# Performance work log

Hardware: AMD Instinct MI355X
Metric: run time of the kernel (lower is better)

## Reference

```python
import jax, jax.numpy as jnp
import numpy as np

H, DQS, DQP, DVS, DVP = 12, 16, 4, 16, 8
S_SCALAR = (3.0 * DQS) ** -0.5
S_POINT = (3.0 * DQP * (9.0 * 2.0 ** 0.5)) ** -0.5
S_PAIR = 3.0 ** -0.5
_OFF = np.cumsum([0, H * DQS, H * DQS, H * DVS, H * DQP * 3, H * DQP * 3, H * DVP * 3])


def _ln(x, g, b, eps=1e-5):
    mu = x.mean(-1, keepdims=True)
    var = x.var(-1, keepdims=True)
    return (x - mu) / jnp.sqrt(var + eps) * g + b


def setup_inputs() -> dict:
    B, N, D, PD = 2, 512, 384, 128
    key = jax.random.key(0)
    ks = jax.random.split(key, 12)
    node_feats = jax.random.normal(ks[0], (B, N, D), jnp.float32)
    pair_feats = jax.random.normal(ks[1], (B, N, N, PD), jnp.float32)
    mask = jnp.ones((B, N), dtype=bool)
    # random per-residue rigid frames (orthonormal rotations via QR)
    rot = jnp.linalg.qr(jax.random.normal(ks[2], (B, N, 3, 3), jnp.float32))[0]
    trans = jax.random.normal(ks[3], (B, N, 3), jnp.float32)
    dim_qkv = int(_OFF[-1])             # 1152
    dim_out = H * (PD + DVS + 4 * DVP)  # 2112
    s = 0.02
    p = dict(
        ln_s_g=jnp.ones((D,)), ln_s_b=jnp.zeros((D,)),
        ln_p_g=jnp.ones((PD,)), ln_p_b=jnp.zeros((PD,)),
        w_pair_bias=s * jax.random.normal(ks[4], (PD, H), jnp.float32),
        w_qkv=s * jax.random.normal(ks[5], (D, dim_qkv), jnp.float32),
        point_weights=jnp.full((1, H, 1, 1), float(np.log(np.e - 1.0)), jnp.float32),
        w_out=s * jax.random.normal(ks[6], (dim_out, D), jnp.float32),
        b_out=jnp.zeros((D,)),
        ln_t_g=jnp.ones((D,)), ln_t_b=jnp.zeros((D,)),
        w_ff1=s * jax.random.normal(ks[7], (D, 4 * D), jnp.float32),
        b_ff1=jnp.zeros((4 * D,)),
        w_ff2=s * jax.random.normal(ks[8], (4 * D, D), jnp.float32),
        b_ff2=jnp.zeros((D,)),
    )
    return dict(node_feats=node_feats, pair_feats=pair_feats, mask=mask,
                rot=rot, trans=trans, **p)


def reference(node_feats, pair_feats, mask, rot, trans,
              ln_s_g, ln_s_b, ln_p_g, ln_p_b, w_pair_bias, w_qkv,
              point_weights, w_out, b_out,
              ln_t_g, ln_t_b, w_ff1, b_ff1, w_ff2, b_ff2):
    b, n, d = node_feats.shape
    x = _ln(node_feats, ln_s_g, ln_s_b)
    p = _ln(pair_feats, ln_p_g, ln_p_b)
    pair_bias = jnp.einsum('bijd,dh->bhij', p, w_pair_bias)
    qkv = x @ w_qkv  # (b,n,1152)

    def heads(t, dh):
        return t.reshape(b, n, H, dh).transpose(0, 2, 1, 3)  # b h n d

    q_s = heads(qkv[..., _OFF[0]:_OFF[1]], DQS)
    k_s = heads(qkv[..., _OFF[1]:_OFF[2]], DQS)
    v_s = heads(qkv[..., _OFF[2]:_OFF[3]], DVS)

    def to_pts(t, dp):
        pts = t.reshape(b, n, H * dp, 3)
        # rigid apply: R_i @ x + t_i (global frame)
        pts = jnp.einsum('bnxy,bnpy->bnpx', rot, pts) + trans[:, :, None, :]
        return pts.reshape(b, n, H, dp, 3).transpose(0, 2, 1, 3, 4)  # b h n d 3

    q_p = to_pts(qkv[..., _OFF[3]:_OFF[4]], DQP)
    k_p = to_pts(qkv[..., _OFF[4]:_OFF[5]], DQP)
    v_p = to_pts(qkv[..., _OFF[5]:_OFF[6]], DVP)

    scalar_logits = jnp.einsum('bhid,bhjd->bhij', q_s, k_s)
    # dist attn: -sum_{d,c} (q-k)^2, expanded to avoid (b,h,n,n,d,3) intermediate
    qq = jnp.sum(q_p * q_p, axis=(-1, -2))
    kk = jnp.sum(k_p * k_p, axis=(-1, -2))
    qk = jnp.einsum('bhidc,bhjdc->bhij', q_p, k_p)
    point_logits = -(qq[..., :, None] + kk[..., None, :] - 2.0 * qk)
    point_logits = point_logits * jax.nn.softplus(point_weights)

    neg = jnp.finfo(node_feats.dtype).min
    pm = mask[:, None, :, None] & mask[:, None, None, :]  # b 1 i j
    scalar_logits = jnp.where(pm, scalar_logits, neg)
    point_logits = jnp.where(pm, point_logits, neg)
    pair_bias = jnp.where(pm, pair_bias, neg)

    logits = S_SCALAR * scalar_logits + S_POINT * point_logits + S_PAIR * pair_bias
    attn = jax.nn.softmax(logits, axis=-1)

    out_s = jnp.einsum('bhij,bhjd->bhid', attn, v_s)
    out_pair = jnp.einsum('bhij,bijd->bhid', attn, p)
    out_p = jnp.einsum('bhij,bhjdc->bhidc', attn, v_p)
    # rigid inverse: R_i^T (x - t_i) back to local frame
    pts = out_p.transpose(0, 2, 1, 3, 4).reshape(b, n, H * DVP, 3)
    pts = jnp.einsum('bnyx,bnpy->bnpx', rot, pts - trans[:, :, None, :])
    out_p = pts.reshape(b, n, H, DVP, 3)
    pnorm = jnp.sqrt(jnp.sum(out_p * out_p, axis=-1) + 1e-8)  # safe_norm

    cat = jnp.concatenate([
        out_s.transpose(0, 2, 1, 3).reshape(b, n, H * DVS),
        out_p.reshape(b, n, H * DVP * 3),
        pnorm.reshape(b, n, H * DVP),
        out_pair.transpose(0, 2, 1, 3).reshape(b, n, -1),
    ], axis=-1)
    attn_out = cat @ w_out + b_out

    # residuals + transition (dropout=0 -> identity). Note: transition is
    # applied to attn_out (pre-residual), exactly as in the torch forward.
    node1 = attn_out + node_feats
    t = _ln(attn_out, ln_t_g, ln_t_b)
    t = jax.nn.gelu(t @ w_ff1 + b_ff1) @ w_ff2 + b_ff2
    return t + node1
```

## Files before the change

### kernel.cpp

```cpp
#include <hip/hip_runtime.h>
#include <hip/hip_bf16.h>
#include <math.h>

typedef __hip_bfloat16 bf16;
typedef _Float16 f16;
typedef unsigned short ushort_t;
typedef ushort_t ushort8 __attribute__((ext_vector_type(8)));
typedef ushort_t us4 __attribute__((ext_vector_type(4)));
typedef short bf16x8 __attribute__((ext_vector_type(8)));
typedef f16 f16x8 __attribute__((ext_vector_type(8)));
typedef float f32x4 __attribute__((ext_vector_type(4)));

constexpr float S_SCALAR = 0.14433756729740643f;
constexpr float S_POINT  = 0.08091531528f;
constexpr float S_PAIR   = 0.5773502691896258f;

__device__ inline float ldf(const float* p) { return *p; }
__device__ inline void stf(float* p, float v) { *p = v; }

__device__ inline short f2bfs(float x) {
  return (short)__builtin_bit_cast(unsigned short, __float2bfloat16(x));
}
__device__ inline ushort_t f2bfu(float x) {
  return (ushort_t)__builtin_bit_cast(unsigned short, __float2bfloat16(x));
}
__device__ inline ushort_t f2hu(float x) {
  return __builtin_bit_cast(ushort_t, (f16)x);
}
__device__ inline float h2f(ushort_t u) {
  return (float)__builtin_bit_cast(f16, u);
}

__device__ inline float gelu_tanh(float x) {
  float c = 0.7978845608028654f * (x + 0.044715f * x * x * x);
  return 0.5f * x * (1.f + tanhf(c));
}

__global__ __launch_bounds__(128) void ln384_kernel(
    const float* __restrict__ in, const float* __restrict__ g,
    const float* __restrict__ b, float* __restrict__ out)
{
  int row = blockIdx.x;
  const float* x = in + (size_t)row * 384;
  int t = threadIdx.x;
  float v[3]; float s = 0.f, s2 = 0.f;
#pragma unroll
  for (int i = 0; i < 3; i++) { v[i] = x[t + 128 * i]; s += v[i]; s2 += v[i] * v[i]; }
  for (int o = 32; o; o >>= 1) { s += __shfl_down(s, o); s2 += __shfl_down(s2, o); }
  __shared__ float sh[4];
  int wid = t >> 6, lane = t & 63;
  if (lane == 0) { sh[wid] = s; sh[2 + wid] = s2; }
  __syncthreads();
  s = sh[0] + sh[1]; s2 = sh[2] + sh[3];
  float mean = s * (1.f / 384.f);
  float var = s2 * (1.f / 384.f) - mean * mean;
  float rstd = rsqrtf(fmaxf(var, 0.f) + 1e-5f);
  float* orow = out + (size_t)row * 384;
#pragma unroll
  for (int i = 0; i < 3; i++) {
    int c = t + 128 * i;
    orow[c] = (v[i] - mean) * rstd * g[c] + b[c];
  }
}

__global__ __launch_bounds__(256) void prep_all_kernel(
    const float* __restrict__ w_qkv, const float* __restrict__ w_out,
    const float* __restrict__ w_ff1, const float* __restrict__ w_ff2,
    ushort_t* __restrict__ wqkvT, ushort_t* __restrict__ woutT,
    ushort_t* __restrict__ wff1T, ushort_t* __restrict__ wff2T,
    const float* __restrict__ g, const float* __restrict__ bb,
    const float* __restrict__ wpb, ushort_t* __restrict__ gwbT,
    float* __restrict__ gsbs,
    const float* __restrict__ node, const float* __restrict__ ln_s_g,
    const float* __restrict__ ln_s_b, float* __restrict__ xout)
{
  __shared__ float shmem[2048];
  int bid = blockIdx.x;
  int t = threadIdx.x;
  if (bid < 2376) {
    const float* src; ushort_t* dst; int K, N, bx, by;
    if (bid < 432)       { src = w_qkv; dst = wqkvT; K = 384;  N = 1152; bx = bid % 36;          by = bid / 36; }
    else if (bid < 1224) { src = w_out; dst = woutT; K = 2112; N = 384;  bx = (bid - 432) % 12;  by = (bid - 432) / 12; }
    else if (bid < 1800) { src = w_ff1; dst = wff1T; K = 384;  N = 1536; bx = (bid - 1224) % 48; by = (bid - 1224) / 48; }
    else                 { src = w_ff2; dst = wff2T; K = 1536; N = 384;  bx = (bid - 1800) % 12; by = (bid - 1800) / 12; }
    float (&tile)[32][33] = *reinterpret_cast<float (*)[32][33]>(shmem);
    int n0 = bx * 32, k0 = by * 32;
    int c = t & 31, r4 = (t >> 5) * 4;
#pragma unroll
    for (int i = 0; i < 4; i++)
      tile[r4 + i][c] = src[(size_t)(k0 + r4 + i) * N + n0 + c];
    __syncthreads();
#pragma unroll
    for (int i = 0; i < 4; i++)
      dst[(size_t)(n0 + r4 + i) * K + k0 + c] = f2bfu(tile[c][r4 + i]);
    return;
  }
  if (bid == 2376) {
    for (int idx = t; idx < 2048; idx += 256) {
      int h = idx >> 7, c = idx & 127;
      float v = (h < 12) ? g[c] * wpb[c * 12 + h] : 0.f;
      bf16 r = __float2bfloat16(v);
      gwbT[idx] = __builtin_bit_cast(unsigned short, r);
      shmem[idx] = __bfloat162float(r);
    }
    __syncthreads();
    if (t < 16) {
      float s = 0.f;
      for (int c = 0; c < 128; c++) s += shmem[t * 128 + c];
      gsbs[t] = s;
    } else if (t < 32) {
      int h = t - 16;
      float s = 0.f;
      if (h < 12) for (int c = 0; c < 128; c++) s = fmaf(bb[c], wpb[c * 12 + h], s);
      gsbs[t] = s;
    }
    return;
  }
  int half = t >> 7, tt = t & 127;
  int row = (bid - 2377) * 2 + half;
  const float* x = node + (size_t)row * 384;
  float v[3]; float s = 0.f, s2 = 0.f;
#pragma unroll
  for (int i = 0; i < 3; i++) { v[i] = x[tt + 128 * i]; s += v[i]; s2 += v[i] * v[i]; }
  for (int o = 32; o; o >>= 1) { s += __shfl_down(s, o); s2 += __shfl_down(s2, o); }
  int wid = t >> 6, lane = t & 63;
  if (lane == 0) { shmem[wid] = s; shmem[4 + wid] = s2; }
  __syncthreads();
  s = shmem[half * 2] + shmem[half * 2 + 1];
  s2 = shmem[4 + half * 2] + shmem[4 + half * 2 + 1];
  float mean = s * (1.f / 384.f);
  float var = s2 * (1.f / 384.f) - mean * mean;
  float rstd = rsqrtf(fmaxf(var, 0.f) + 1e-5f);
  float* orow = xout + (size_t)row * 384;
#pragma unroll
  for (int i = 0; i < 3; i++) {
    int c = tt + 128 * i;
    orow[c] = (v[i] - mean) * rstd * ln_s_g[c] + ln_s_b[c];
  }
}

template <int EPI>
__global__ __launch_bounds__(256) void gemm_mfma_kernel(
    const float* __restrict__ A, const ushort_t* __restrict__ BT,
    const float* __restrict__ bias, const float* __restrict__ r1,
    const float* __restrict__ r2, float* __restrict__ C,
    int M, int Nn, int K)
{
  __shared__ ushort_t As[64][72];
  __shared__ ushort_t Bs[64][72];
  int t = threadIdx.x;
  int w = t >> 6, l = t & 63;
  int m0 = blockIdx.y * 64, n0 = blockIdx.x * 64;
  int wm = (w >> 1) * 32, wn = (w & 1) * 32;
  int lr = l & 15, lk = l >> 4;
  int sr = t >> 2, sc = (t & 3) * 16;
  f32x4 acc[2][2];
#pragma unroll
  for (int i = 0; i < 2; i++)
#pragma unroll
    for (int j = 0; j < 2; j++) acc[i][j] = (f32x4){0.f, 0.f, 0.f, 0.f};

  for (int k0 = 0; k0 < K; k0 += 64) {
    const float* Ar = A + (size_t)(m0 + sr) * K + k0 + sc;
    const ushort_t* Br = BT + (size_t)(n0 + sr) * K + k0 + sc;
    float4 a0 = *(const float4*)(Ar + 0);
    float4 a1 = *(const float4*)(Ar + 4);
    float4 a2 = *(const float4*)(Ar + 8);
    float4 a3 = *(const float4*)(Ar + 12);
    ushort8 b0 = *(const ushort8*)(Br + 0);
    ushort8 b1 = *(const ushort8*)(Br + 8);
    ushort8 u0, u1;
    u0[0] = f2bfu(a0.x); u0[1] = f2bfu(a0.y); u0[2] = f2bfu(a0.z); u0[3] = f2bfu(a0.w);
    u0[4] = f2bfu(a1.x); u0[5] = f2bfu(a1.y); u0[6] = f2bfu(a1.z); u0[7] = f2bfu(a1.w);
    u1[0] = f2bfu(a2.x); u1[1] = f2bfu(a2.y); u1[2] = f2bfu(a2.z); u1[3] = f2bfu(a2.w);
    u1[4] = f2bfu(a3.x); u1[5] = f2bfu(a3.y); u1[6] = f2bfu(a3.z); u1[7] = f2bfu(a3.w);
    *(ushort8*)&As[sr][sc] = u0;
    *(ushort8*)&As[sr][sc + 8] = u1;
    *(ushort8*)&Bs[sr][sc] = b0;
    *(ushort8*)&Bs[sr][sc + 8] = b1;
    __syncthreads();
#pragma unroll
    for (int kk = 0; kk < 2; kk++) {
      bf16x8 af0 = *(const bf16x8*)&As[wm + lr][kk * 32 + lk * 8];
      bf16x8 af1 = *(const bf16x8*)&As[wm + 16 + lr][kk * 32 + lk * 8];
      bf16x8 bf0 = *(const bf16x8*)&Bs[wn + lr][kk * 32 + lk * 8];
      bf16x8 bf1 = *(const bf16x8*)&Bs[wn + 16 + lr][kk * 32 + lk * 8];
      acc[0][0] = __builtin_amdgcn_mfma_f32_16x16x32_bf16(af0, bf0, acc[0][0], 0, 0, 0);
      acc[0][1] = __builtin_amdgcn_mfma_f32_16x16x32_bf16(af0, bf1, acc[0][1], 0, 0, 0);
      acc[1][0] = __builtin_amdgcn_mfma_f32_16x16x32_bf16(af1, bf0, acc[1][0], 0, 0, 0);
      acc[1][1] = __builtin_amdgcn_mfma_f32_16x16x32_bf16(af1, bf1, acc[1][1], 0, 0, 0);
    }
    __syncthreads();
  }
#pragma unroll
  for (int mf = 0; mf < 2; mf++) {
#pragma unroll
    for (int nf = 0; nf < 2; nf++) {
      int nn = n0 + wn + nf * 16 + lr;
      float bv = bias ? bias[nn] : 0.f;
#pragma unroll
      for (int e = 0; e < 4; e++) {
        int m = m0 + wm + mf * 16 + lk * 4 + e;
        float v = acc[mf][nf][e] + bv;
        if (EPI == 1) v = gelu_tanh(v);
        if (EPI == 2) v += r1[(size_t)m * Nn + nn] + r2[(size_t)m * Nn + nn];
        C[(size_t)m * Nn + nn] = v;
      }
    }
  }
}

__global__ __launch_bounds__(256) void qkv_post_kernel(
    const float* __restrict__ qkv, const float* __restrict__ rot,
    const float* __restrict__ trans, const float* __restrict__ pw,
    f16* __restrict__ qhat, f16* __restrict__ khat,
    float* __restrict__ kkb, ushort_t* __restrict__ vT)
{
  int bh = blockIdx.x;
  int b = bh / 12, h = bh - b * 12;
  int j = blockIdx.y * 256 + threadIdx.x;
  int bn = b * 512 + j;
  const float* row = qkv + (size_t)bn * 1152;
  float R[9];
#pragma unroll
  for (int k = 0; k < 9; k++) R[k] = rot[bn * 9 + k];
  float T0 = trans[bn * 3], T1 = trans[bn * 3 + 1], T2 = trans[bn * 3 + 2];
  float sp = log1pf(__expf(pw[h]));
  float c1 = 2.f * S_POINT * sp;
  f16* qh = qhat + ((size_t)bh * 512 + j) * 32;
  f16* kh = khat + ((size_t)bh * 512 + j) * 32;
#pragma unroll
  for (int d = 0; d < 16; d++) {
    qh[d] = (f16)(S_SCALAR * row[h * 16 + d]);
    kh[d] = (f16)(row[192 + h * 16 + d]);
  }
#pragma unroll
  for (int p = 0; p < 4; p++) {
    int base = 576 + (h * 4 + p) * 3;
    float x = row[base], y = row[base + 1], z = row[base + 2];
    qh[16 + p * 3 + 0] = (f16)(c1 * (R[0] * x + R[1] * y + R[2] * z + T0));
    qh[16 + p * 3 + 1] = (f16)(c1 * (R[3] * x + R[4] * y + R[5] * z + T1));
    qh[16 + p * 3 + 2] = (f16)(c1 * (R[6] * x + R[7] * y + R[8] * z + T2));
  }
  float kksum = 0.f;
#pragma unroll
  for (int p = 0; p < 4; p++) {
    int base = 720 + (h * 4 + p) * 3;
    float x = row[base], y = row[base + 1], z = row[base + 2];
    float gx = R[0] * x + R[1] * y + R[2] * z + T0;
    float gy = R[3] * x + R[4] * y + R[5] * z + T1;
    float gz = R[6] * x + R[7] * y + R[8] * z + T2;
    kh[16 + p * 3 + 0] = (f16)gx; kh[16 + p * 3 + 1] = (f16)gy; kh[16 + p * 3 + 2] = (f16)gz;
    kksum = fmaf(gx, gx, kksum); kksum = fmaf(gy, gy, kksum); kksum = fmaf(gz, gz, kksum);
  }
#pragma unroll
  for (int d = 28; d < 32; d++) { qh[d] = (f16)0.f; kh[d] = (f16)0.f; }
  kkb[(size_t)bh * 512 + j] = kksum;
  ushort_t* vt = vT + (size_t)bh * 40 * 512;
#pragma unroll
  for (int c = 0; c < 16; c++) vt[c * 512 + j] = f2hu(row[384 + h * 16 + c]);
#pragma unroll
  for (int p = 0; p < 8; p++) {
    int base = 864 + (h * 8 + p) * 3;
    float x = row[base], y = row[base + 1], z = row[base + 2];
    vt[(16 + p * 3 + 0) * 512 + j] = f2hu(R[0] * x + R[1] * y + R[2] * z + T0);
    vt[(16 + p * 3 + 1) * 512 + j] = f2hu(R[3] * x + R[4] * y + R[5] * z + T1);
    vt[(16 + p * 3 + 2) * 512 + j] = f2hu(R[6] * x + R[7] * y + R[8] * z + T2);
  }
}

__global__ __launch_bounds__(256) void pair_bias_kernel(
    const float* __restrict__ pair, const ushort_t* __restrict__ gwbT,
    const float* __restrict__ gsbs, const float* __restrict__ g,
    const float* __restrict__ bb, ushort_t* __restrict__ bias,
    f16* __restrict__ pnT)
{
  int t = threadIdx.x;
  int wv = t >> 6, l = t & 63;
  int lr = l & 15, lk = l >> 4;
  size_t rid0 = (size_t)blockIdx.x * 128 + (size_t)wv * 32;

  bf16x8 bfrag[4];
#pragma unroll
  for (int kc = 0; kc < 4; kc++) {
    const ushort_t* gp = gwbT + lr * 128 + kc * 32 + lk * 8;
    us4 q0 = *(const us4*)gp;
    us4 q1 = *(const us4*)(gp + 4);
    bfrag[kc][0] = (short)q0[0]; bfrag[kc][1] = (short)q0[1];
    bfrag[kc][2] = (short)q0[2]; bfrag[kc][3] = (short)q0[3];
    bfrag[kc][4] = (short)q1[0]; bfrag[kc][5] = (short)q1[1];
    bfrag[kc][6] = (short)q1[2]; bfrag[kc][7] = (short)q1[3];
  }

  const float* p0 = pair + (rid0 + lr) * 128 + lk * 8;
  f32x4 acc0 = {0.f, 0.f, 0.f, 0.f}, acc1 = {0.f, 0.f, 0.f, 0.f};
  float s0 = 0.f, s20 = 0.f, s1 = 0.f, s21 = 0.f;
#pragma unroll
  for (int kc = 0; kc < 4; kc++) {
    float4 u0 = *(const float4*)(p0 + kc * 32);
    float4 u1 = *(const float4*)(p0 + kc * 32 + 4);
    float4 w0 = *(const float4*)(p0 + 2048 + kc * 32);
    float4 w1 = *(const float4*)(p0 + 2048 + kc * 32 + 4);
    s0 += u0.x + u0.y + u0.z + u0.w + u1.x + u1.y + u1.z + u1.w;
    s20 = fmaf(u0.x, u0.x, s20); s20 = fmaf(u0.y, u0.y, s20);
    s20 = fmaf(u0.z, u0.z, s20); s20 = fmaf(u0.w, u0.w, s20);
    s20 = fmaf(u1.x, u1.x, s20); s20 = fmaf(u1.y, u1.y, s20);
    s20 = fmaf(u1.z, u1.z, s20); s20 = fmaf(u1.w, u1.w, s20);
    s1 += w0.x + w0.y + w0.z + w0.w + w1.x + w1.y + w1.z + w1.w;
    s21 = fmaf(w0.x, w0.x, s21); s21 = fmaf(w0.y, w0.y, s21);
    s21 = fmaf(w0.z, w0.z, s21); s21 = fmaf(w0.w, w0.w, s21);
    s21 = fmaf(w1.x, w1.x, s21); s21 = fmaf(w1.y, w1.y, s21);
    s21 = fmaf(w1.z, w1.z, s21); s21 = fmaf(w1.w, w1.w, s21);
    bf16x8 a0, a1;
    a0[0] = f2bfs(u0.x); a0[1] = f2bfs(u0.y); a0[2] = f2bfs(u0.z); a0[3] = f2bfs(u0.w);
    a0[4] = f2bfs(u1.x); a0[5] = f2bfs(u1.y); a0[6] = f2bfs(u1.z); a0[7] = f2bfs(u1.w);
    a1[0] = f2bfs(w0.x); a1[1] = f2bfs(w0.y); a1[2] = f2bfs(w0.z); a1[3] = f2bfs(w0.w);
    a1[4] = f2bfs(w1.x); a1[5] = f2bfs(w1.y); a1[6] = f2bfs(w1.z); a1[7] = f2bfs(w1.w);
    acc0 = __builtin_amdgcn_mfma_f32_16x16x32_bf16(a0, bfrag[kc], acc0, 0, 0, 0);
    acc1 = __builtin_amdgcn_mfma_f32_16x16x32_bf16(a1, bfrag[kc], acc1, 0, 0, 0);
  }
  s0 += __shfl_xor(s0, 16);  s0 += __shfl_xor(s0, 32);
  s20 += __shfl_xor(s20, 16); s20 += __shfl_xor(s20, 32);
  s1 += __shfl_xor(s1, 16);  s1 += __shfl_xor(s1, 32);
  s21 += __shfl_xor(s21, 16); s21 += __shfl_xor(s21, 32);
  float mean0 = s0 * (1.f / 128.f);
  float rstd0 = rsqrtf(fmaxf(s20 * (1.f / 128.f) - mean0 * mean0, 0.f) + 1e-5f);
  float mean1 = s1 * (1.f / 128.f);
  float rstd1 = rsqrtf(fmaxf(s21 * (1.f / 128.f) - mean1 * mean1, 0.f) + 1e-5f);

  int slab = (int)(rid0 >> 9);
  int j0w = (int)(rid0 & 511);
  f16* sl = pnT + (size_t)slab * 65536;
  int ju = j0w + lr, jw = j0w + 16 + lr;
#pragma unroll
  for (int kc = 0; kc < 4; kc++) {
    int c0 = kc * 32 + lk * 8;
    float4 u0 = *(const float4*)(p0 + kc * 32);
    float4 u1 = *(const float4*)(p0 + kc * 32 + 4);
    float4 w0 = *(const float4*)(p0 + 2048 + kc * 32);
    float4 w1 = *(const float4*)(p0 + 2048 + kc * 32 + 4);
    float4 g0 = *(const float4*)(g + c0);
    float4 g1 = *(const float4*)(g + c0 + 4);
    float4 b0 = *(const float4*)(bb + c0);
    float4 b1 = *(const float4*)(bb + c0 + 4);
    float uu[8] = {u0.x, u0.y, u0.z, u0.w, u1.x, u1.y, u1.z, u1.w};
    float ww[8] = {w0.x, w0.y, w0.z, w0.w, w1.x, w1.y, w1.z, w1.w};
    float gg[8] = {g0.x, g0.y, g0.z, g0.w, g1.x, g1.y, g1.z, g1.w};
    float bv[8] = {b0.x, b0.y, b0.z, b0.w, b1.x, b1.y, b1.z, b1.w};
#pragma unroll
    for (int e = 0; e < 8; e++) {
      sl[(size_t)(c0 + e) * 512 + ju] = (f16)(fmaf((uu[e] - mean0) * rstd0, gg[e], bv[e]));
      sl[(size_t)(c0 + e) * 512 + jw] = (f16)(fmaf((ww[e] - mean1) * rstd1, gg[e], bv[e]));
    }
  }

  float gsum = gsbs[lr], bsum = gsbs[16 + lr];
  int b = (int)(rid0 >> 18);
  int i = (int)((rid0 >> 9) & 511);
  int j0 = (int)(rid0 & 511);
  us4 pk0, pk1;
#pragma unroll
  for (int e = 0; e < 4; e++) {
    int r = lk * 4 + e;
    float m0 = __shfl(mean0, r), rs0 = __shfl(rstd0, r);
    float m1 = __shfl(mean1, r), rs1 = __shfl(rstd1, r);
    pk0[e] = f2hu(rs0 * (acc0[e] - m0 * gsum) + bsum);
    pk1[e] = f2hu(rs1 * (acc1[e] - m1 * gsum) + bsum);
  }
  if (lr < 12) {
    ushort_t* dst = bias + ((size_t)(b * 12 + lr) * 512 + i) * 512 + j0 + lk * 4;
    *(us4*)dst = pk0;
    *(us4*)(dst + 16) = pk1;
  }
}

__global__ __launch_bounds__(256, 1) void attn_kernel(
    const f16* __restrict__ qhat, const f16* __restrict__ khat,
    const float* __restrict__ kkb, const ushort_t* __restrict__ bias,
    const float* __restrict__ pw, ushort_t* __restrict__ attn)
{
  int i0 = blockIdx.x * 64;
  int bh = blockIdx.y;
  int b = bh / 12, h = bh - b * 12;
  int t = threadIdx.x;
  int w = t >> 6, l = t & 63, lr = l & 15, lk = l >> 4;
  float spp = S_POINT * log1pf(__expf(pw[h]));
  int iw0 = i0 + w * 16;
  f16x8 afrag = *(const f16x8*)(qhat + ((size_t)bh * 512 + iw0 + lr) * 32 + lk * 8);
  const f16* kbase = khat + (size_t)bh * 512 * 32;
  const float* kkrow = kkb + (size_t)bh * 512;
  const ushort_t* brow = bias + (size_t)bh * 512 * 512;
  float lg[32][4];
  float pmax[4] = {-3.0e38f, -3.0e38f, -3.0e38f, -3.0e38f};
#pragma unroll
  for (int jt = 0; jt < 32; jt++) {
    int j = jt * 16 + lr;
    f16x8 bfrag = *(const f16x8*)(kbase + (size_t)j * 32 + lk * 8);
    f32x4 c = {0.f, 0.f, 0.f, 0.f};
    c = __builtin_amdgcn_mfma_f32_16x16x32_f16(afrag, bfrag, c, 0, 0, 0);
    float kkv = kkrow[j];
#pragma unroll
    for (int e = 0; e < 4; e++) {
      int i = iw0 + lk * 4 + e;
      float lv = c[e] + S_PAIR * h2f(brow[(size_t)i * 512 + j]) - spp * kkv;
      lg[jt][e] = lv;
      pmax[e] = fmaxf(pmax[e], lv);
    }
  }
#pragma unroll
  for (int e = 0; e < 4; e++) {
    pmax[e] = fmaxf(pmax[e], __shfl_xor(pmax[e], 1));
    pmax[e] = fmaxf(pmax[e], __shfl_xor(pmax[e], 2));
    pmax[e] = fmaxf(pmax[e], __shfl_xor(pmax[e], 4));
    pmax[e] = fmaxf(pmax[e], __shfl_xor(pmax[e], 8));
  }
  float ssum[4] = {0.f, 0.f, 0.f, 0.f};
#pragma unroll
  for (int jt = 0; jt < 32; jt++)
#pragma unroll
    for (int e = 0; e < 4; e++) {
      float p = __expf(lg[jt][e] - pmax[e]);
      lg[jt][e] = p;
      ssum[e] += p;
    }
#pragma unroll
  for (int e = 0; e < 4; e++) {
    ssum[e] += __shfl_xor(ssum[e], 1);
    ssum[e] += __shfl_xor(ssum[e], 2);
    ssum[e] += __shfl_xor(ssum[e], 4);
    ssum[e] += __shfl_xor(ssum[e], 8);
    ssum[e] = 1.f / ssum[e];
  }
#pragma unroll
  for (int jt = 0; jt < 32; jt++)
#pragma unroll
    for (int e = 0; e < 4; e++) {
      int i = iw0 + lk * 4 + e;
      attn[((size_t)(b * 512 + i) * 12 + h) * 512 + jt * 16 + lr] = f2hu(lg[jt][e] * ssum[e]);
    }
}

__global__ __launch_bounds__(256) void sv_gemm_kernel(
    const ushort_t* __restrict__ attn, const ushort_t* __restrict__ vT,
    float* __restrict__ svraw)
{
  int i0 = blockIdx.x * 64;
  int bh = blockIdx.y;
  int b = bh / 12, h = bh - b * 12;
  __shared__ ushort_t As_[64][72];
  __shared__ ushort_t Bs_[48][72];
  int t = threadIdx.x;
  int w = t >> 6, l = t & 63, lr = l & 15, lk = l >> 4;
  int ai = t >> 2, as = (t & 3) * 16;
  const ushort_t* vbase = vT + (size_t)bh * 40 * 512;
  f32x4 acc[3];
#pragma unroll
  for (int n = 0; n < 3; n++) acc[n] = (f32x4){0.f, 0.f, 0.f, 0.f};

  for (int jt = 0; jt < 8; jt++) {
    int jb = jt * 64;
    size_t aoff = ((size_t)(b * 512 + i0 + ai) * 12 + h) * 512 + jb + as;
    ushort8 a0 = *(const ushort8*)(attn + aoff);
    ushort8 a1 = *(const ushort8*)(attn + aoff + 8);
    *(ushort8*)&As_[ai][as] = a0;
    *(ushort8*)&As_[ai][as + 8] = a1;
    for (int idx = t; idx < 384; idx += 256) {
      int c = idx >> 3, j8 = (idx & 7) * 8;
      ushort8 v = {0, 0, 0, 0, 0, 0, 0, 0};
      if (c < 40) v = *(const ushort8*)(vbase + (size_t)c * 512 + jb + j8);
      *(ushort8*)&Bs_[c][j8] = v;
    }
    __syncthreads();
#pragma unroll
    for (int kk = 0; kk < 2; kk++) {
      f16x8 af = *(const f16x8*)&As_[w * 16 + lr][kk * 32 + lk * 8];
#pragma unroll
      for (int n = 0; n < 3; n++) {
        f16x8 bf_ = *(const f16x8*)&Bs_[n * 16 + lr][kk * 32 + lk * 8];
        acc[n] = __builtin_amdgcn_mfma_f32_16x16x32_f16(af, bf_, acc[n], 0, 0, 0);
      }
    }
    __syncthreads();
  }
#pragma unroll
  for (int n = 0; n < 3; n++) {
    int c = n * 16 + lr;
    if (c < 40) {
#pragma unroll
      for (int e = 0; e < 4; e++) {
        int i = i0 + w * 16 + lk * 4 + e;
        svraw[(size_t)(b * 512 + i) * 480 + h * 40 + c] = acc[n][e];
      }
    }
  }
}

__global__ __launch_bounds__(256) void pair_out_kernel(
    const ushort_t* __restrict__ attn, const f16* __restrict__ pnT,
    const float* __restrict__ svraw, const float* __restrict__ rot,
    const float* __restrict__ trans, float* __restrict__ cat)
{
  int bn = blockIdx.x;
  int t = threadIdx.x;
  const float* sv = svraw + (size_t)bn * 480;
  float* crow = cat + (size_t)bn * 2112;
  if (t < 192) {
    int h2 = t >> 4, d = t & 15;
    crow[t] = sv[h2 * 40 + d];
    if (t < 96) {
      int h3 = t >> 3, dp = t & 7;
      float T0 = trans[bn * 3], T1 = trans[bn * 3 + 1], T2 = trans[bn * 3 + 2];
      const float* R = rot + bn * 9;
      float px = sv[h3 * 40 + 16 + dp * 3 + 0] - T0;
      float py = sv[h3 * 40 + 16 + dp * 3 + 1] - T1;
      float pz = sv[h3 * 40 + 16 + dp * 3 + 2] - T2;
      float lx = R[0] * px + R[3] * py + R[6] * pz;
      float ly = R[1] * px + R[4] * py + R[7] * pz;
      float lz = R[2] * px + R[5] * py + R[8] * pz;
      crow[192 + h3 * 24 + dp * 3 + 0] = lx;
      crow[192 + h3 * 24 + dp * 3 + 1] = ly;
      crow[192 + h3 * 24 + dp * 3 + 2] = lz;
      crow[480 + h3 * 8 + dp] = sqrtf(lx * lx + ly * ly + lz * lz + 1e-8f);
    }
  }
  int w = t >> 6, l = t & 63, lr = l & 15, lk = l >> 4;
  const ushort_t* arow = attn + (size_t)bn * 12 * 512;
  int ar = (lr < 12) ? lr : 11;
  const f16* slab = pnT + (size_t)bn * 65536;
  int n0 = w * 32;
  f32x4 acc0 = {0.f, 0.f, 0.f, 0.f}, acc1 = {0.f, 0.f, 0.f, 0.f};
#pragma unroll
  for (int ks = 0; ks < 16; ks++) {
    int kb = ks * 32 + lk * 8;
    f16x8 af = *(const f16x8*)((const f16*)arow + (size_t)ar * 512 + kb);
    f16x8 b0 = *(const f16x8*)(slab + (size_t)(n0 + lr) * 512 + kb);
    f16x8 b1 = *(const f16x8*)(slab + (size_t)(n0 + 16 + lr) * 512 + kb);
    acc0 = __builtin_amdgcn_mfma_f32_16x16x32_f16(af, b0, acc0, 0, 0, 0);
    acc1 = __builtin_amdgcn_mfma_f32_16x16x32_f16(af, b1, acc1, 0, 0, 0);
  }
#pragma unroll
  for (int e = 0; e < 4; e++) {
    int hh = lk * 4 + e;
    if (hh < 12) {
      crow[576 + hh * 128 + n0 + lr] = acc0[e];
      crow[576 + hh * 128 + n0 + 16 + lr] = acc1[e];
    }
  }
}

extern "C" void kernel_launch(void* const* d_in, const int* in_sizes, int n_in,
                              void* d_out, int out_size, void* d_ws, size_t ws_size,
                              hipStream_t stream)
{
  const float* node   = (const float*)d_in[0];
  const float* pair   = (const float*)d_in[1];
  const float* rot    = (const float*)d_in[3];
  const float* trans  = (const float*)d_in[4];
  const float* ln_s_g = (const float*)d_in[5];
  const float* ln_s_b = (const float*)d_in[6];
  const float* ln_p_g = (const float*)d_in[7];
  const float* ln_p_b = (const float*)d_in[8];
  const float* wpb    = (const float*)d_in[9];
  const float* w_qkv  = (const float*)d_in[10];
  const float* pw     = (const float*)d_in[11];
  const float* w_out  = (const float*)d_in[12];
  const float* b_out  = (const float*)d_in[13];
  const float* ln_t_g = (const float*)d_in[14];
  const float* ln_t_b = (const float*)d_in[15];
  const float* w_ff1  = (const float*)d_in[16];
  const float* b_ff1  = (const float*)d_in[17];
  const float* w_ff2  = (const float*)d_in[18];
  const float* b_ff2  = (const float*)d_in[19];
  float* out = (float*)d_out;
  float* ws = (float*)d_ws;

  float* qkv    = ws;
  float* x      = ws + 1179648;
  float* tn     = x;
  float* ao     = ws + 1572864;
  float* svraw  = ws + 1966080;
  ushort_t* biasb = (ushort_t*)(ws + 2457600);
  float* cat    = ws + 2457600;
  ushort_t* attnb = (ushort_t*)(ws + 5603328);
  float* gb     = ws + 5603328;
  ushort_t* gwbT = (ushort_t*)(ws + 8749056);
  float* gsbs   = ws + 8750080;
  ushort_t* wqkvT = (ushort_t*)(ws + 8750112);
  ushort_t* woutT = (ushort_t*)(ws + 8971296);
  ushort_t* wff1T = (ushort_t*)(ws + 9376800);
  ushort_t* wff2T = (ushort_t*)(ws + 9671712);
  f16* qhat     = (f16*)(ws + 9966624);
  f16* khat     = (f16*)(ws + 10163232);
  float* kkb    = ws + 10359840;
  ushort_t* vT  = (ushort_t*)(ws + 10372128);
  f16* pnT      = (f16*)(ws + 10617888);

  prep_all_kernel<<<2889, 256, 0, stream>>>(w_qkv, w_out, w_ff1, w_ff2,
      wqkvT, woutT, wff1T, wff2T, ln_p_g, ln_p_b, wpb, gwbT, gsbs,
      node, ln_s_g, ln_s_b, x);
  gemm_mfma_kernel<0><<<dim3(18, 16), 256, 0, stream>>>(x, wqkvT, nullptr, nullptr, nullptr, qkv, 1024, 1152, 384);
  qkv_post_kernel<<<dim3(24, 2), 256, 0, stream>>>(qkv, rot, trans, pw, qhat, khat, kkb, vT);
  pair_bias_kernel<<<4096, 256, 0, stream>>>(pair, gwbT, gsbs, ln_p_g, ln_p_b, biasb, pnT);
  attn_kernel<<<dim3(8, 24), 256, 0, stream>>>(qhat, khat, kkb, biasb, pw, attnb);
  sv_gemm_kernel<<<dim3(8, 24), 256, 0, stream>>>(attnb, vT, svraw);
  pair_out_kernel<<<1024, 256, 0, stream>>>(attnb, pnT, svraw, rot, trans, cat);
  gemm_mfma_kernel<0><<<dim3(6, 16), 256, 0, stream>>>(cat, woutT, b_out, nullptr, nullptr, ao, 1024, 384, 2112);
  ln384_kernel<<<1024, 128, 0, stream>>>(ao, ln_t_g, ln_t_b, tn);
  gemm_mfma_kernel<1><<<dim3(24, 16), 256, 0, stream>>>(tn, wff1T, b_ff1, nullptr, nullptr, gb, 1024, 1536, 384);
  gemm_mfma_kernel<2><<<dim3(6, 16), 256, 0, stream>>>(gb, wff2T, b_ff2, ao, node, out, 1024, 384, 1536);
}
```

Baseline: 632.8 us.

## Coalesce pnT and attention stores, split qkv_post roles, add M32 GEMM

```diff
diff --git a/kernel.cpp b/kernel.cpp
--- a/kernel.cpp
+++ b/kernel.cpp
@@ -14,9 +14,6 @@
 constexpr float S_SCALAR = 0.14433756729740643f;
 constexpr float S_POINT  = 0.08091531528f;
 constexpr float S_PAIR   = 0.5773502691896258f;
-
-__device__ inline float ldf(const float* p) { return *p; }
-__device__ inline void stf(float* p, float v) { *p = v; }
 
 __device__ inline short f2bfs(float x) {
   return (short)__builtin_bit_cast(unsigned short, __float2bfloat16(x));
@@ -210,6 +207,63 @@
   }
 }
 
+template <int EPI>
+__global__ __launch_bounds__(256) void gemm_mfma_m32_kernel(
+    const float* __restrict__ A, const ushort_t* __restrict__ BT,
+    const float* __restrict__ bias, const float* __restrict__ r1,
+    const float* __restrict__ r2, float* __restrict__ C,
+    int M, int Nn, int K)
+{
+  __shared__ ushort_t As[32][72];
+  __shared__ ushort_t Bs[64][72];
+  int t = threadIdx.x;
+  int w = t >> 6, l = t & 63;
+  int m0 = blockIdx.y * 32, n0 = blockIdx.x * 64;
+  int wm = (w & 1) * 16, wn = (w >> 1) * 32;
+  int lr = l & 15, lk = l >> 4;
+  int ar = t >> 3, ac = (t & 7) * 8;
+  int br = t >> 2, bc = (t & 3) * 16;
+  f32x4 acc[2];
+  acc[0] = (f32x4){0.f, 0.f, 0.f, 0.f};
+  acc[1] = (f32x4){0.f, 0.f, 0.f, 0.f};
+
+  for (int k0 = 0; k0 < K; k0 += 64) {
+    const float* Ar = A + (size_t)(m0 + ar) * K + k0 + ac;
+    float4 a0 = *(const float4*)(Ar + 0);
+    float4 a1 = *(const float4*)(Ar + 4);
+    ushort8 u;
+    u[0] = f2bfu(a0.x); u[1] = f2bfu(a0.y); u[2] = f2bfu(a0.z); u[3] = f2bfu(a0.w);
+    u[4] = f2bfu(a1.x); u[5] = f2bfu(a1.y); u[6] = f2bfu(a1.z); u[7] = f2bfu(a1.w);
+    *(ushort8*)&As[ar][ac] = u;
+    const ushort_t* Br = BT + (size_t)(n0 + br) * K + k0 + bc;
+    *(ushort8*)&Bs[br][bc] = *(const ushort8*)(Br + 0);
+    *(ushort8*)&Bs[br][bc + 8] = *(const ushort8*)(Br + 8);
+    __syncthreads();
+#pragma unroll
+    for (int kk = 0; kk < 2; kk++) {
+      bf16x8 af = *(const bf16x8*)&As[wm + lr][kk * 32 + lk * 8];
+      bf16x8 bf0 = *(const bf16x8*)&Bs[wn + lr][kk * 32 + lk * 8];
+      bf16x8 bf1 = *(const bf16x8*)&Bs[wn + 16 + lr][kk * 32 + lk * 8];
+      acc[0] = __builtin_amdgcn_mfma_f32_16x16x32_bf16(af, bf0, acc[0], 0, 0, 0);
+      acc[1] = __builtin_amdgcn_mfma_f32_16x16x32_bf16(af, bf1, acc[1], 0, 0, 0);
+    }
+    __syncthreads();
+  }
+#pragma unroll
+  for (int nf = 0; nf < 2; nf++) {
+    int nn = n0 + wn + nf * 16 + lr;
+    float bv = bias ? bias[nn] : 0.f;
+#pragma unroll
+    for (int e = 0; e < 4; e++) {
+      int m = m0 + wm + lk * 4 + e;
+      float v = acc[nf][e] + bv;
+      if (EPI == 1) v = gelu_tanh(v);
+      if (EPI == 2) v += r1[(size_t)m * Nn + nn] + r2[(size_t)m * Nn + nn];
+      C[(size_t)m * Nn + nn] = v;
+    }
+  }
+}
+
 __global__ __launch_bounds__(256) void qkv_post_kernel(
     const float* __restrict__ qkv, const float* __restrict__ rot,
     const float* __restrict__ trans, const float* __restrict__ pw,
@@ -218,54 +272,60 @@
 {
   int bh = blockIdx.x;
   int b = bh / 12, h = bh - b * 12;
-  int j = blockIdx.y * 256 + threadIdx.x;
+  int role = blockIdx.y >> 1;
+  int j = (blockIdx.y & 1) * 256 + threadIdx.x;
   int bn = b * 512 + j;
   const float* row = qkv + (size_t)bn * 1152;
   float R[9];
 #pragma unroll
   for (int k = 0; k < 9; k++) R[k] = rot[bn * 9 + k];
   float T0 = trans[bn * 3], T1 = trans[bn * 3 + 1], T2 = trans[bn * 3 + 2];
-  float sp = log1pf(__expf(pw[h]));
-  float c1 = 2.f * S_POINT * sp;
-  f16* qh = qhat + ((size_t)bh * 512 + j) * 32;
-  f16* kh = khat + ((size_t)bh * 512 + j) * 32;
-#pragma unroll
-  for (int d = 0; d < 16; d++) {
-    qh[d] = (f16)(S_SCALAR * row[h * 16 + d]);
-    kh[d] = (f16)(row[192 + h * 16 + d]);
-  }
-#pragma unroll
-  for (int p = 0; p < 4; p++) {
-    int base = 576 + (h * 4 + p) * 3;
-    float x = row[base], y = row[base + 1], z = row[base + 2];
-    qh[16 + p * 3 + 0] = (f16)(c1 * (R[0] * x + R[1] * y + R[2] * z + T0));
-    qh[16 + p * 3 + 1] = (f16)(c1 * (R[3] * x + R[4] * y + R[5] * z + T1));
-    qh[16 + p * 3 + 2] = (f16)(c1 * (R[6] * x + R[7] * y + R[8] * z + T2));
-  }
-  float kksum = 0.f;
-#pragma unroll
-  for (int p = 0; p < 4; p++) {
-    int base = 720 + (h * 4 + p) * 3;
-    float x = row[base], y = row[base + 1], z = row[base + 2];
-    float gx = R[0] * x + R[1] * y + R[2] * z + T0;
-    float gy = R[3] * x + R[4] * y + R[5] * z + T1;
-    float gz = R[6] * x + R[7] * y + R[8] * z + T2;
-    kh[16 + p * 3 + 0] = (f16)gx; kh[16 + p * 3 + 1] = (f16)gy; kh[16 + p * 3 + 2] = (f16)gz;
-    kksum = fmaf(gx, gx, kksum); kksum = fmaf(gy, gy, kksum); kksum = fmaf(gz, gz, kksum);
-  }
-#pragma unroll
-  for (int d = 28; d < 32; d++) { qh[d] = (f16)0.f; kh[d] = (f16)0.f; }
-  kkb[(size_t)bh * 512 + j] = kksum;
-  ushort_t* vt = vT + (size_t)bh * 40 * 512;
-#pragma unroll
-  for (int c = 0; c < 16; c++) vt[c * 512 + j] = f2hu(row[384 + h * 16 + c]);
-#pragma unroll
-  for (int p = 0; p < 8; p++) {
-    int base = 864 + (h * 8 + p) * 3;
-    float x = row[base], y = row[base + 1], z = row[base + 2];
-    vt[(16 + p * 3 + 0) * 512 + j] = f2hu(R[0] * x + R[1] * y + R[2] * z + T0);
-    vt[(16 + p * 3 + 1) * 512 + j] = f2hu(R[3] * x + R[4] * y + R[5] * z + T1);
-    vt[(16 + p * 3 + 2) * 512 + j] = f2hu(R[6] * x + R[7] * y + R[8] * z + T2);
+  if (role == 0) {
+    float sp = log1pf(__expf(pw[h]));
+    float c1 = 2.f * S_POINT * sp;
+    f16* qh = qhat + ((size_t)bh * 512 + j) * 32;
+#pragma unroll
+    for (int d = 0; d < 16; d++) qh[d] = (f16)(S_SCALAR * row[h * 16 + d]);
+#pragma unroll
+    for (int p = 0; p < 4; p++) {
+      int base = 576 + (h * 4 + p) * 3;
+      float x = row[base], y = row[base + 1], z = row[base + 2];
+      qh[16 + p * 3 + 0] = (f16)(c1 * (R[0] * x + R[1] * y + R[2] * z + T0));
+      qh[16 + p * 3 + 1] = (f16)(c1 * (R[3] * x + R[4] * y + R[5] * z + T1));
+      qh[16 + p * 3 + 2] = (f16)(c1 * (R[6] * x + R[7] * y + R[8] * z + T2));
+    }
+#pragma unroll
+    for (int d = 28; d < 32; d++) qh[d] = (f16)0.f;
+  } else if (role == 1) {
+    f16* kh = khat + ((size_t)bh * 512 + j) * 32;
+#pragma unroll
+    for (int d = 0; d < 16; d++) kh[d] = (f16)(row[192 + h * 16 + d]);
+    float kksum = 0.f;
+#pragma unroll
+    for (int p = 0; p < 4; p++) {
+      int base = 720 + (h * 4 + p) * 3;
+      float x = row[base], y = row[base + 1], z = row[base + 2];
+      float gx = R[0] * x + R[1] * y + R[2] * z + T0;
+      float gy = R[3] * x + R[4] * y + R[5] * z + T1;
+      float gz = R[6] * x + R[7] * y + R[8] * z + T2;
+      kh[16 + p * 3 + 0] = (f16)gx; kh[16 + p * 3 + 1] = (f16)gy; kh[16 + p * 3 + 2] = (f16)gz;
+      kksum = fmaf(gx, gx, kksum); kksum = fmaf(gy, gy, kksum); kksum = fmaf(gz, gz, kksum);
+    }
+#pragma unroll
+    for (int d = 28; d < 32; d++) kh[d] = (f16)0.f;
+    kkb[(size_t)bh * 512 + j] = kksum;
+  } else {
+    ushort_t* vt = vT + (size_t)bh * 40 * 512;
+#pragma unroll
+    for (int c = 0; c < 16; c++) vt[c * 512 + j] = f2hu(row[384 + h * 16 + c]);
+#pragma unroll
+    for (int p = 0; p < 8; p++) {
+      int base = 864 + (h * 8 + p) * 3;
+      float x = row[base], y = row[base + 1], z = row[base + 2];
+      vt[(16 + p * 3 + 0) * 512 + j] = f2hu(R[0] * x + R[1] * y + R[2] * z + T0);
+      vt[(16 + p * 3 + 1) * 512 + j] = f2hu(R[3] * x + R[4] * y + R[5] * z + T1);
+      vt[(16 + p * 3 + 2) * 512 + j] = f2hu(R[6] * x + R[7] * y + R[8] * z + T2);
+    }
   }
 }
 
@@ -275,6 +335,7 @@
     const float* __restrict__ bb, ushort_t* __restrict__ bias,
     f16* __restrict__ pnT)
 {
+  __shared__ ushort_t tile[128][136];
   int t = threadIdx.x;
   int wv = t >> 6, l = t & 63;
   int lr = l & 15, lk = l >> 4;
@@ -328,10 +389,7 @@
   float mean1 = s1 * (1.f / 128.f);
   float rstd1 = rsqrtf(fmaxf(s21 * (1.f / 128.f) - mean1 * mean1, 0.f) + 1e-5f);
 
-  int slab = (int)(rid0 >> 9);
-  int j0w = (int)(rid0 & 511);
-  f16* sl = pnT + (size_t)slab * 65536;
-  int ju = j0w + lr, jw = j0w + 16 + lr;
+  int jl_u = wv * 32 + lr, jl_w = wv * 32 + 16 + lr;
 #pragma unroll
   for (int kc = 0; kc < 4; kc++) {
     int c0 = kc * 32 + lk * 8;
@@ -349,8 +407,24 @@
     float bv[8] = {b0.x, b0.y, b0.z, b0.w, b1.x, b1.y, b1.z, b1.w};
 #pragma unroll
     for (int e = 0; e < 8; e++) {
-      sl[(size_t)(c0 + e) * 512 + ju] = (f16)(fmaf((uu[e] - mean0) * rstd0, gg[e], bv[e]));
-      sl[(size_t)(c0 + e) * 512 + jw] = (f16)(fmaf((ww[e] - mean1) * rstd1, gg[e], bv[e]));
+      int c = c0 + e;
+      int sw = ((c >> 3) & 7) << 4;
+      tile[c][jl_u ^ sw] = f2hu(fmaf((uu[e] - mean0) * rstd0, gg[e], bv[e]));
+      tile[c][jl_w ^ sw] = f2hu(fmaf((ww[e] - mean1) * rstd1, gg[e], bv[e]));
+    }
+  }
+  __syncthreads();
+  {
+    int slab = blockIdx.x >> 2;
+    int j0blk = (blockIdx.x & 3) * 128;
+    ushort_t* dstb = (ushort_t*)pnT + (size_t)slab * 65536 + j0blk;
+#pragma unroll
+    for (int it = 0; it < 8; it++) {
+      int idx = t + 256 * it;
+      int c = idx >> 4, o = idx & 15;
+      int sw = ((c >> 3) & 7) << 4;
+      ushort8 v = *(const ushort8*)&tile[c][(o * 8) ^ sw];
+      *(ushort8*)(dstb + (size_t)c * 512 + o * 8) = v;
     }
   }
 
@@ -385,59 +459,50 @@
   int t = threadIdx.x;
   int w = t >> 6, l = t & 63, lr = l & 15, lk = l >> 4;
   float spp = S_POINT * log1pf(__expf(pw[h]));
-  int iw0 = i0 + w * 16;
-  f16x8 afrag = *(const f16x8*)(qhat + ((size_t)bh * 512 + iw0 + lr) * 32 + lk * 8);
+  int i = i0 + w * 16 + lr;
+  f16x8 bfrag = *(const f16x8*)(qhat + ((size_t)bh * 512 + i) * 32 + lk * 8);
   const f16* kbase = khat + (size_t)bh * 512 * 32;
   const float* kkrow = kkb + (size_t)bh * 512;
-  const ushort_t* brow = bias + (size_t)bh * 512 * 512;
+  const ushort_t* brow = bias + ((size_t)bh * 512 + i) * 512;
   float lg[32][4];
-  float pmax[4] = {-3.0e38f, -3.0e38f, -3.0e38f, -3.0e38f};
+  float pmax = -3.0e38f;
 #pragma unroll
   for (int jt = 0; jt < 32; jt++) {
-    int j = jt * 16 + lr;
-    f16x8 bfrag = *(const f16x8*)(kbase + (size_t)j * 32 + lk * 8);
+    f16x8 afrag = *(const f16x8*)(kbase + (size_t)(jt * 16 + lr) * 32 + lk * 8);
     f32x4 c = {0.f, 0.f, 0.f, 0.f};
     c = __builtin_amdgcn_mfma_f32_16x16x32_f16(afrag, bfrag, c, 0, 0, 0);
-    float kkv = kkrow[j];
+    us4 bq = *(const us4*)(brow + jt * 16 + lk * 4);
+    float4 kq = *(const float4*)(kkrow + jt * 16 + lk * 4);
+    float kk4[4] = {kq.x, kq.y, kq.z, kq.w};
 #pragma unroll
     for (int e = 0; e < 4; e++) {
-      int i = iw0 + lk * 4 + e;
-      float lv = c[e] + S_PAIR * h2f(brow[(size_t)i * 512 + j]) - spp * kkv;
+      float lv = c[e] + S_PAIR * h2f(bq[e]) - spp * kk4[e];
       lg[jt][e] = lv;
-      pmax[e] = fmaxf(pmax[e], lv);
-    }
-  }
-#pragma unroll
-  for (int e = 0; e < 4; e++) {
-    pmax[e] = fmaxf(pmax[e], __shfl_xor(pmax[e], 1));
-    pmax[e] = fmaxf(pmax[e], __shfl_xor(pmax[e], 2));
-    pmax[e] = fmaxf(pmax[e], __shfl_xor(pmax[e], 4));
-    pmax[e] = fmaxf(pmax[e], __shfl_xor(pmax[e], 8));
-  }
-  float ssum[4] = {0.f, 0.f, 0.f, 0.f};
+      pmax = fmaxf(pmax, lv);
+    }
+  }
+  pmax = fmaxf(pmax, __shfl_xor(pmax, 16));
+  pmax = fmaxf(pmax, __shfl_xor(pmax, 32));
+  float ssum = 0.f;
 #pragma unroll
   for (int jt = 0; jt < 32; jt++)
 #pragma unroll
     for (int e = 0; e < 4; e++) {
-      float p = __expf(lg[jt][e] - pmax[e]);
+      float p = __expf(lg[jt][e] - pmax);
       lg[jt][e] = p;
-      ssum[e] += p;
-    }
-#pragma unroll
-  for (int e = 0; e < 4; e++) {
-    ssum[e] += __shfl_xor(ssum[e], 1);
-    ssum[e] += __shfl_xor(ssum[e], 2);
-    ssum[e] += __shfl_xor(ssum[e], 4);
-    ssum[e] += __shfl_xor(ssum[e], 8);
-    ssum[e] = 1.f / ssum[e];
-  }
-#pragma unroll
-  for (int jt = 0; jt < 32; jt++)
-#pragma unroll
-    for (int e = 0; e < 4; e++) {
-      int i = iw0 + lk * 4 + e;
-      attn[((size_t)(b * 512 + i) * 12 + h) * 512 + jt * 16 + lr] = f2hu(lg[jt][e] * ssum[e]);
-    }
+      ssum += p;
+    }
+  ssum += __shfl_xor(ssum, 16);
+  ssum += __shfl_xor(ssum, 32);
+  float inv = 1.f / ssum;
+  ushort_t* arow = attn + ((size_t)(b * 512 + i) * 12 + h) * 512;
+#pragma unroll
+  for (int jt = 0; jt < 32; jt++) {
+    us4 o;
+#pragma unroll
+    for (int e = 0; e < 4; e++) o[e] = f2hu(lg[jt][e] * inv);
+    *(us4*)(arow + jt * 16 + lk * 4) = o;
+  }
 }
 
 __global__ __launch_bounds__(256) void sv_gemm_kernel(
@@ -599,13 +664,13 @@
       wqkvT, woutT, wff1T, wff2T, ln_p_g, ln_p_b, wpb, gwbT, gsbs,
       node, ln_s_g, ln_s_b, x);
   gemm_mfma_kernel<0><<<dim3(18, 16), 256, 0, stream>>>(x, wqkvT, nullptr, nullptr, nullptr, qkv, 1024, 1152, 384);
-  qkv_post_kernel<<<dim3(24, 2), 256, 0, stream>>>(qkv, rot, trans, pw, qhat, khat, kkb, vT);
+  qkv_post_kernel<<<dim3(24, 6), 256, 0, stream>>>(qkv, rot, trans, pw, qhat, khat, kkb, vT);
   pair_bias_kernel<<<4096, 256, 0, stream>>>(pair, gwbT, gsbs, ln_p_g, ln_p_b, biasb, pnT);
   attn_kernel<<<dim3(8, 24), 256, 0, stream>>>(qhat, khat, kkb, biasb, pw, attnb);
   sv_gemm_kernel<<<dim3(8, 24), 256, 0, stream>>>(attnb, vT, svraw);
   pair_out_kernel<<<1024, 256, 0, stream>>>(attnb, pnT, svraw, rot, trans, cat);
-  gemm_mfma_kernel<0><<<dim3(6, 16), 256, 0, stream>>>(cat, woutT, b_out, nullptr, nullptr, ao, 1024, 384, 2112);
+  gemm_mfma_m32_kernel<0><<<dim3(6, 32), 256, 0, stream>>>(cat, woutT, b_out, nullptr, nullptr, ao, 1024, 384, 2112);
   ln384_kernel<<<1024, 128, 0, stream>>>(ao, ln_t_g, ln_t_b, tn);
   gemm_mfma_kernel<1><<<dim3(24, 16), 256, 0, stream>>>(tn, wff1T, b_ff1, nullptr, nullptr, gb, 1024, 1536, 384);
-  gemm_mfma_kernel<2><<<dim3(6, 16), 256, 0, stream>>>(gb, wff2T, b_ff2, ao, node, out, 1024, 384, 1536);
-}
+  gemm_mfma_m32_kernel<2><<<dim3(6, 32), 256, 0, stream>>>(gb, wff2T, b_ff2, ao, node, out, 1024, 384, 1536);
+}
```

After: 587.6 us. -7.1%, faster.
